# Performance work log

Measured on AMD Instinct MI355X. Metric: run time of the kernel, lower is better.

The kernel has to match this reference:

```python
import jax, jax.numpy as jnp
import numpy as np

N_NODES = 50000
N_EDGES = 625000
N_GRAPHS = 256
D = 128
STEPS = 3


def setup_inputs() -> dict:
    key = jax.random.key(0)
    ks = jax.random.split(key, 12)
    x = jax.random.normal(ks[0], (N_NODES, D), dtype=jnp.float32)
    edge_index = jax.random.randint(ks[1], (2, N_EDGES), 0, N_NODES, dtype=jnp.int64)
    batch = jnp.sort(jax.random.randint(ks[2], (N_NODES,), 0, N_GRAPHS, dtype=jnp.int64))
    s = 1.0 / np.sqrt(D)
    W1 = jax.random.uniform(ks[3], (D, D), jnp.float32, -s, s)
    b1 = jnp.zeros((D,), jnp.float32)
    W2 = jax.random.uniform(ks[4], (D, D), jnp.float32, -s, s)
    b2 = jnp.zeros((D,), jnp.float32)
    sh = 1.0 / np.sqrt(D)  # hidden size = D
    Wih = jax.random.uniform(ks[5], (4 * D, 2 * D), jnp.float32, -sh, sh)
    Whh = jax.random.uniform(ks[6], (4 * D, D), jnp.float32, -sh, sh)
    bih = jax.random.uniform(ks[7], (4 * D,), jnp.float32, -sh, sh)
    bhh = jax.random.uniform(ks[8], (4 * D,), jnp.float32, -sh, sh)
    return {"x": x, "edge_index": edge_index, "batch": batch,
            "W1": W1, "b1": b1, "W2": W2, "b2": b2,
            "Wih": Wih, "Whh": Whh, "bih": bih, "bhh": bhh}


def gcn_conv(x, edge_index, W, b):
    n = x.shape[0]
    src, dst = edge_index[0], edge_index[1]
    deg = jax.ops.segment_sum(jnp.ones(src.shape[0], x.dtype), dst, num_segments=n) + 1.0
    dinv = jax.lax.rsqrt(deg)
    xw = x @ W  # [N, out]
    norm = dinv[src] * dinv[dst]  # [E]
    agg = jax.ops.segment_sum(xw[src] * norm[:, None], dst, num_segments=n)
    agg = agg + xw * (dinv * dinv)[:, None]  # self-loop term (weight 1/deg_i)
    return agg + b


def set2set(x, batch, Wih, Whh, bih, bhh):
    d = x.shape[1]
    B = N_GRAPHS
    h = jnp.zeros((B, d), x.dtype)
    c = jnp.zeros((B, d), x.dtype)
    q_star = jnp.zeros((B, 2 * d), x.dtype)
    for _ in range(STEPS):
        # single-layer LSTM step (torch gate order: i, f, g, o)
        gates = q_star @ Wih.T + bih + h @ Whh.T + bhh
        i, f, g, o = jnp.split(gates, 4, axis=-1)
        c = jax.nn.sigmoid(f) * c + jax.nn.sigmoid(i) * jnp.tanh(g)
        h = jax.nn.sigmoid(o) * jnp.tanh(c)
        q = h  # [B, d]
        # attention with segment softmax over nodes grouped by graph
        e = jnp.sum(x * q[batch], axis=-1)  # [N]
        m = jax.ops.segment_max(e, batch, num_segments=B)
        m = jnp.where(jnp.isfinite(m), m, 0.0)  # guard empty graphs
        ex = jnp.exp(e - m[batch])
        ssum = jax.ops.segment_sum(ex, batch, num_segments=B)
        a = ex / (ssum[batch] + 1e-16)
        r = jax.ops.segment_sum(a[:, None] * x, batch, num_segments=B)  # [B, d]
        q_star = jnp.concatenate([q, r], axis=-1)
    return q_star  # [B, 2d]


def reference(x, edge_index, batch, W1, b1, W2, b2, Wih, Whh, bih, bhh):
    h1 = jax.nn.relu(gcn_conv(x, edge_index, W1, b1))
    h2 = gcn_conv(h1, edge_index, W2, b2)
    return set2set(h2, batch, Wih, Whh, bih, bhh)
```

## Files before the change

### kernel.cpp

```cpp
#include <hip/hip_runtime.h>
#include <hip/hip_fp16.h>
#include <math.h>

#define D 128

__device__ __forceinline__ float sigmoidf_(float x) { return 1.0f / (1.0f + expf(-x)); }

__global__ void k_deg(const int* __restrict__ dst, int* __restrict__ cnt, int E) {
    int i = blockIdx.x * blockDim.x + threadIdx.x;
    if (i < E) atomicAdd(&cnt[dst[i]], 1);
}

__global__ __launch_bounds__(256) void k_scan1(const int* __restrict__ cnt, int* __restrict__ row_ptr,
                                               int* __restrict__ bsum, float* __restrict__ dinv,
                                               int* __restrict__ fillc, int N) {
    __shared__ int sh[256];
    int t = threadIdx.x;
    int i = blockIdx.x * 256 + t;
    int v = (i < N) ? cnt[i] : 0;
    if (i < N) {
        dinv[i] = rsqrtf((float)v + 1.0f);
        fillc[i] = 0;
    }
    sh[t] = v;
    __syncthreads();
    for (int off = 1; off < 256; off <<= 1) {
        int u = (t >= off) ? sh[t - off] : 0;
        __syncthreads();
        sh[t] += u;
        __syncthreads();
    }
    if (i < N) row_ptr[i] = sh[t] - v;
    if (t == 255) bsum[blockIdx.x] = sh[255];
}

__global__ __launch_bounds__(256) void k_scan2(int* __restrict__ bsum, int nb,
                                               const int* __restrict__ batch, int* __restrict__ gstart,
                                               int N, int G) {
    __shared__ int sh[256];
    int t = threadIdx.x;
    int v = (t < nb) ? bsum[t] : 0;
    sh[t] = v;
    __syncthreads();
    for (int off = 1; off < 256; off <<= 1) {
        int u = (t >= off) ? sh[t - off] : 0;
        __syncthreads();
        sh[t] += u;
        __syncthreads();
    }
    if (t < nb) bsum[t] = sh[t] - v;
    for (int g = t; g <= G; g += 256) {
        int lo = 0, hi = N;
        while (lo < hi) {
            int mid = (lo + hi) >> 1;
            if (batch[mid] < g) lo = mid + 1; else hi = mid;
        }
        gstart[g] = lo;
    }
}

__global__ __launch_bounds__(256) void k_scan3(int* __restrict__ row_ptr, const int* __restrict__ bsum,
                                               int N, int E) {
    int i = blockIdx.x * 256 + threadIdx.x;
    if (i < N) row_ptr[i] += bsum[blockIdx.x];
    if (i == 0) row_ptr[N] = E;
}

__global__ void k_fill(const int* __restrict__ src, const int* __restrict__ dst,
                       const int* __restrict__ row_ptr, int* __restrict__ fillc,
                       int* __restrict__ s_sorted, int E) {
    int i = blockIdx.x * blockDim.x + threadIdx.x;
    if (i >= E) return;
    int s = src[i], d = dst[i];
    int pos = row_ptr[d] + atomicAdd(&fillc[d], 1);
    s_sorted[pos] = s;
}

__global__ __launch_bounds__(256) void k_prepw(const float* __restrict__ Wih, const float* __restrict__ Whh,
                                               float* __restrict__ Wcomb) {
    __shared__ float ta[32][33], tb[32][33];
    int t = threadIdx.x;
    int tx = t & 31, ty = t >> 5;
    int bk = blockIdx.x & 7, bj = blockIdx.x >> 3;
    int k0 = bk * 32, j0 = bj * 32;
    bool hh = (k0 < 128);
#pragma unroll
    for (int i = 0; i < 32; i += 8) ta[ty + i][tx] = Wih[(size_t)(j0 + ty + i) * 256 + k0 + tx];
    if (hh) {
#pragma unroll
        for (int i = 0; i < 32; i += 8) tb[ty + i][tx] = Whh[(size_t)(j0 + ty + i) * 128 + k0 + tx];
    }
    __syncthreads();
#pragma unroll
    for (int i = 0; i < 32; i += 8) {
        float v = ta[tx][ty + i];
        if (hh) v += tb[tx][ty + i];
        Wcomb[(size_t)(k0 + ty + i) * 512 + j0 + tx] = v;
    }
}

__global__ __launch_bounds__(256) void k_gemm(const float* __restrict__ X, const float* __restrict__ W,
                                              const float* __restrict__ dinv, __half* __restrict__ Y, int M) {
    __shared__ float Xs[32][68];
    __shared__ float Ws[32][128];
    int block_row = blockIdx.x * 64;
    int tid = threadIdx.x;
    int trr = tid >> 4;
    int tc = tid & 15;
    float acc[4][8] = {};
    for (int k0 = 0; k0 < 128; k0 += 32) {
        for (int i = tid; i < 512; i += 256) {
            int r = i >> 3, kk = (i & 7) << 2;
            int row = block_row + r;
            float4 v = make_float4(0.f, 0.f, 0.f, 0.f);
            if (row < M) v = *(const float4*)&X[(size_t)row * D + k0 + kk];
            Xs[kk + 0][r] = v.x; Xs[kk + 1][r] = v.y; Xs[kk + 2][r] = v.z; Xs[kk + 3][r] = v.w;
        }
        for (int i = tid; i < 1024; i += 256) {
            int r = i >> 5, cc = (i & 31) << 2;
            *(float4*)&Ws[r][cc] = *(const float4*)&W[(size_t)(k0 + r) * D + cc];
        }
        __syncthreads();
#pragma unroll
        for (int k = 0; k < 32; ++k) {
            float4 xv = *(const float4*)&Xs[k][trr * 4];
            float4 w0 = *(const float4*)&Ws[k][tc * 4];
            float4 w1 = *(const float4*)&Ws[k][tc * 4 + 64];
            float xr[4] = {xv.x, xv.y, xv.z, xv.w};
            float wc[8] = {w0.x, w0.y, w0.z, w0.w, w1.x, w1.y, w1.z, w1.w};
#pragma unroll
            for (int r = 0; r < 4; ++r)
#pragma unroll
                for (int c = 0; c < 8; ++c)
                    acc[r][c] += xr[r] * wc[c];
        }
        __syncthreads();
    }
    for (int r = 0; r < 4; ++r) {
        int row = block_row + trr * 4 + r;
        if (row < M) {
            float s = dinv[row];
            __half2* y0 = (__half2*)&Y[(size_t)row * D + tc * 4];
            y0[0] = __floats2half2_rn(acc[r][0] * s, acc[r][1] * s);
            y0[1] = __floats2half2_rn(acc[r][2] * s, acc[r][3] * s);
            __half2* y1 = (__half2*)&Y[(size_t)row * D + 64 + tc * 4];
            y1[0] = __floats2half2_rn(acc[r][4] * s, acc[r][5] * s);
            y1[1] = __floats2half2_rn(acc[r][6] * s, acc[r][7] * s);
        }
    }
}

template <bool RELU>
__global__ __launch_bounds__(256) void k_agg(const __half* __restrict__ xw, const int* __restrict__ s_sorted,
                                             const int* __restrict__ row_ptr, const float* __restrict__ dinv,
                                             const float* __restrict__ bias, float* __restrict__ out, int N) {
    int n = blockIdx.x * 4 + (threadIdx.x >> 6);
    if (n >= N) return;
    int l = threadIdx.x & 63;
    int beg = row_ptr[n], end = row_ptr[n + 1];
    float2 a[8];
#pragma unroll
    for (int k = 0; k < 8; ++k) a[k] = make_float2(0.f, 0.f);
    for (int e = beg; e < end; e += 8) {
#pragma unroll
        for (int k = 0; k < 8; ++k) {
            int idx = e + k;
            int ee = min(idx, end - 1);
            int s = s_sorted[ee];
            __half2 hv = *(const __half2*)&xw[(size_t)s * D + 2 * l];
            float2 xv = __half22float2(hv);
            bool ok = (idx < end);
            a[k].x += ok ? xv.x : 0.f;
            a[k].y += ok ? xv.y : 0.f;
        }
    }
    float din = dinv[n];
    __half2 hself = *(const __half2*)&xw[(size_t)n * D + 2 * l];
    float2 xs = __half22float2(hself);
    float2 bv = *(const float2*)&bias[2 * l];
    float sx = ((a[0].x + a[1].x) + (a[2].x + a[3].x)) + ((a[4].x + a[5].x) + (a[6].x + a[7].x));
    float sy = ((a[0].y + a[1].y) + (a[2].y + a[3].y)) + ((a[4].y + a[5].y) + (a[6].y + a[7].y));
    float rx = (sx + xs.x) * din + bv.x;
    float ry = (sy + xs.y) * din + bv.y;
    if (RELU) { rx = fmaxf(rx, 0.f); ry = fmaxf(ry, 0.f); }
    *(float2*)&out[(size_t)n * D + 2 * l] = make_float2(rx, ry);
}

__global__ __launch_bounds__(256) void k_lstm_gemm(const float* __restrict__ q_star,
                                                   const float* __restrict__ Wcomb,
                                                   float* __restrict__ gates) {
    __shared__ float Xs[32][68];
    __shared__ float Ws[32][64];
    int tid = threadIdx.x;
    int bm = blockIdx.x & 3, bn = blockIdx.x >> 2;
    int m0 = bm * 64, n0 = bn * 64;
    int trr = tid >> 4;
    int tc = tid & 15;
    float acc[4][4] = {};
    for (int k0 = 0; k0 < 256; k0 += 32) {
        for (int i = tid; i < 512; i += 256) {
            int r = i >> 3, kk = (i & 7) << 2;
            float4 v = *(const float4*)&q_star[(size_t)(m0 + r) * 256 + k0 + kk];
            Xs[kk + 0][r] = v.x; Xs[kk + 1][r] = v.y; Xs[kk + 2][r] = v.z; Xs[kk + 3][r] = v.w;
        }
        for (int i = tid; i < 512; i += 256) {
            int r = i >> 4, c = (i & 15) << 2;
            *(float4*)&Ws[r][c] = *(const float4*)&Wcomb[(size_t)(k0 + r) * 512 + n0 + c];
        }
        __syncthreads();
#pragma unroll
        for (int k = 0; k < 32; ++k) {
            float4 xv = *(const float4*)&Xs[k][trr * 4];
            float4 wv = *(const float4*)&Ws[k][tc * 4];
            float xr[4] = {xv.x, xv.y, xv.z, xv.w};
            float wc[4] = {wv.x, wv.y, wv.z, wv.w};
#pragma unroll
            for (int r = 0; r < 4; ++r)
#pragma unroll
                for (int c = 0; c < 4; ++c)
                    acc[r][c] += xr[r] * wc[c];
        }
        __syncthreads();
    }
#pragma unroll
    for (int r = 0; r < 4; ++r)
        *(float4*)&gates[(size_t)(m0 + trr * 4 + r) * 512 + n0 + tc * 4] =
            make_float4(acc[r][0], acc[r][1], acc[r][2], acc[r][3]);
}

template <bool FIRST>
__global__ __launch_bounds__(512) void k_attn2(const float* __restrict__ h2, const int* __restrict__ gstart,
                                               const float* __restrict__ gates, const float* __restrict__ bih,
                                               const float* __restrict__ bhh, float* __restrict__ c_all,
                                               float* __restrict__ q_star) {
    int g = blockIdx.x;
    int t = threadIdx.x;
    int wid = t >> 6, l = t & 63;
    int s = gstart[g], epos = gstart[g + 1];
    __shared__ float hs[D];
    __shared__ float wmax[8], wsum[8];
    __shared__ float2 racc2[512];
    if (t < D) {
        float ig = bih[t] + bhh[t];
        float fg = bih[t + D] + bhh[t + D];
        float gg = bih[t + 2 * D] + bhh[t + 2 * D];
        float og = bih[t + 3 * D] + bhh[t + 3 * D];
        if (!FIRST) {
            const float* gr = &gates[(size_t)g * 512];
            ig += gr[t]; fg += gr[t + D]; gg += gr[t + 2 * D]; og += gr[t + 3 * D];
        }
        float cprev = FIRST ? 0.f : c_all[g * D + t];
        float cc = sigmoidf_(fg) * cprev + sigmoidf_(ig) * tanhf(gg);
        float hh = sigmoidf_(og) * tanhf(cc);
        c_all[g * D + t] = cc;
        hs[t] = hh;
        q_star[(size_t)g * 2 * D + t] = hh;
    }
    __syncthreads();
    float2 qv = *(const float2*)&hs[2 * l];
    float m = -1e30f;
    float ssum = 0.f;
    float2 a = {0.f, 0.f};
    for (int i = s + wid * 4; i < epos; i += 32) {
        int i0 = i, i1 = min(i + 1, epos - 1), i2 = min(i + 2, epos - 1), i3 = min(i + 3, epos - 1);
        bool v1 = (i + 1 < epos), v2 = (i + 2 < epos), v3 = (i + 3 < epos);
        float2 x0 = *(const float2*)&h2[(size_t)i0 * D + 2 * l];
        float2 x1 = *(const float2*)&h2[(size_t)i1 * D + 2 * l];
        float2 x2 = *(const float2*)&h2[(size_t)i2 * D + 2 * l];
        float2 x3 = *(const float2*)&h2[(size_t)i3 * D + 2 * l];
        float d0 = x0.x * qv.x + x0.y * qv.y;
        float d1 = x1.x * qv.x + x1.y * qv.y;
        float d2 = x2.x * qv.x + x2.y * qv.y;
        float d3 = x3.x * qv.x + x3.y * qv.y;
#pragma unroll
        for (int off = 32; off; off >>= 1) {
            d0 += __shfl_xor(d0, off);
            d1 += __shfl_xor(d1, off);
            d2 += __shfl_xor(d2, off);
            d3 += __shfl_xor(d3, off);
        }
        {
            if (d0 > m) { float sc = expf(m - d0); a.x *= sc; a.y *= sc; ssum *= sc; m = d0; }
            float p = expf(d0 - m);
            ssum += p; a.x += p * x0.x; a.y += p * x0.y;
        }
        if (v1) {
            if (d1 > m) { float sc = expf(m - d1); a.x *= sc; a.y *= sc; ssum *= sc; m = d1; }
            float p = expf(d1 - m);
            ssum += p; a.x += p * x1.x; a.y += p * x1.y;
        }
        if (v2) {
            if (d2 > m) { float sc = expf(m - d2); a.x *= sc; a.y *= sc; ssum *= sc; m = d2; }
            float p = expf(d2 - m);
            ssum += p; a.x += p * x2.x; a.y += p * x2.y;
        }
        if (v3) {
            if (d3 > m) { float sc = expf(m - d3); a.x *= sc; a.y *= sc; ssum *= sc; m = d3; }
            float p = expf(d3 - m);
            ssum += p; a.x += p * x3.x; a.y += p * x3.y;
        }
    }
    if (l == 0) wmax[wid] = m;
    __syncthreads();
    float M = wmax[0];
#pragma unroll
    for (int w = 1; w < 8; ++w) M = fmaxf(M, wmax[w]);
    float fac = expf(m - M);
    a.x *= fac; a.y *= fac;
    ssum *= fac;
    if (l == 0) wsum[wid] = ssum;
    racc2[t] = a;
    __syncthreads();
    if (t < 64) {
        float S = 0.f;
#pragma unroll
        for (int w = 0; w < 8; ++w) S += wsum[w];
        float2 r = make_float2(0.f, 0.f);
#pragma unroll
        for (int w = 0; w < 8; ++w) { r.x += racc2[t + 64 * w].x; r.y += racc2[t + 64 * w].y; }
        float inv = 1.0f / (S + 1e-16f);
        q_star[(size_t)g * 2 * D + D + 2 * t] = r.x * inv;
        q_star[(size_t)g * 2 * D + D + 2 * t + 1] = r.y * inv;
    }
}

extern "C" void kernel_launch(void* const* d_in, const int* in_sizes, int n_in,
                              void* d_out, int out_size, void* d_ws, size_t ws_size,
                              hipStream_t stream) {
    const float* x = (const float*)d_in[0];
    const int* ei = (const int*)d_in[1];
    const int* batch = (const int*)d_in[2];
    const float* W1 = (const float*)d_in[3];
    const float* b1 = (const float*)d_in[4];
    const float* W2 = (const float*)d_in[5];
    const float* b2 = (const float*)d_in[6];
    const float* Wih = (const float*)d_in[7];
    const float* Whh = (const float*)d_in[8];
    const float* bih = (const float*)d_in[9];
    const float* bhh = (const float*)d_in[10];

    int N = in_sizes[2];
    int E = in_sizes[1] / 2;
    int G = out_size / (2 * D);
    const int* src = ei;
    const int* dst = ei + E;
    float* xbuf = (float*)d_in[0];
    float* q_star = (float*)d_out;

    float* wsf = (float*)d_ws;
    int* wsi = (int*)d_ws;
    size_t off = 0;
    float* dinv = wsf + off;    off += N;
    int* degcnt = wsi + off;    off += N;
    int* row_ptr = wsi + off;   off += N + 1;
    int* bsum = wsi + off;      off += 256;
    off = (off + 3) & ~(size_t)3;
    int* fillc = wsi + off;     off += N;
    int* s_sorted = wsi + off;  off += E;
    off = (off + 3) & ~(size_t)3;
    __half* bufA16 = (__half*)(wsf + off); off += (size_t)N * D / 2 + 4;
    int* gstart = wsi + off;    off += G + 1;
    off = (off + 3) & ~(size_t)3;
    float* Wcomb = wsf + off;   off += 256 * 512;
    float* gates = wsf + off;   off += (size_t)G * 512;
    float* c_all = wsf + off;   off += (size_t)G * D;

    hipMemsetAsync(degcnt, 0, N * sizeof(int), stream);

    int eb = (E + 255) / 256;
    int nb = (N + 255) / 256;
    k_deg<<<eb, 256, 0, stream>>>(dst, degcnt, E);
    k_scan1<<<nb, 256, 0, stream>>>(degcnt, row_ptr, bsum, dinv, fillc, N);
    k_scan2<<<1, 256, 0, stream>>>(bsum, nb, batch, gstart, N, G);
    k_scan3<<<nb, 256, 0, stream>>>(row_ptr, bsum, N, E);
    k_fill<<<eb, 256, 0, stream>>>(src, dst, row_ptr, fillc, s_sorted, E);
    k_prepw<<<128, 256, 0, stream>>>(Wih, Whh, Wcomb);

    int gb = (N + 63) / 64;
    k_gemm<<<gb, 256, 0, stream>>>(x, W1, dinv, bufA16, N);
    k_agg<true><<<(N + 3) / 4, 256, 0, stream>>>(bufA16, s_sorted, row_ptr, dinv, b1, xbuf, N);
    k_gemm<<<gb, 256, 0, stream>>>(xbuf, W2, dinv, bufA16, N);
    k_agg<false><<<(N + 3) / 4, 256, 0, stream>>>(bufA16, s_sorted, row_ptr, dinv, b2, xbuf, N);

    k_attn2<true><<<G, 512, 0, stream>>>(xbuf, gstart, gates, bih, bhh, c_all, q_star);
    for (int step = 1; step < 3; ++step) {
        k_lstm_gemm<<<32, 256, 0, stream>>>(q_star, Wcomb, gates);
        k_attn2<false><<<G, 512, 0, stream>>>(xbuf, gstart, gates, bih, bhh, c_all, q_star);
    }
}
```

Measured before the change: 350.7 us.

## Store hidden activations in fp16 and reuse atomic rank for CSR fill

```diff
diff --git a/kernel.cpp b/kernel.cpp
--- a/kernel.cpp
+++ b/kernel.cpp
@@ -6,22 +6,26 @@
 
 __device__ __forceinline__ float sigmoidf_(float x) { return 1.0f / (1.0f + expf(-x)); }
 
-__global__ void k_deg(const int* __restrict__ dst, int* __restrict__ cnt, int E) {
+__device__ __forceinline__ float4 load4(const float* p) { return *(const float4*)p; }
+__device__ __forceinline__ float4 load4(const __half* p) {
+    __half2 h0 = *(const __half2*)p;
+    __half2 h1 = *(const __half2*)(p + 2);
+    float2 f0 = __half22float2(h0), f1 = __half22float2(h1);
+    return make_float4(f0.x, f0.y, f1.x, f1.y);
+}
+
+__global__ void k_deg(const int* __restrict__ dst, int* __restrict__ cnt, int* __restrict__ rank, int E) {
     int i = blockIdx.x * blockDim.x + threadIdx.x;
-    if (i < E) atomicAdd(&cnt[dst[i]], 1);
+    if (i < E) rank[i] = atomicAdd(&cnt[dst[i]], 1);
 }
 
 __global__ __launch_bounds__(256) void k_scan1(const int* __restrict__ cnt, int* __restrict__ row_ptr,
-                                               int* __restrict__ bsum, float* __restrict__ dinv,
-                                               int* __restrict__ fillc, int N) {
+                                               int* __restrict__ bsum, float* __restrict__ dinv, int N) {
     __shared__ int sh[256];
     int t = threadIdx.x;
     int i = blockIdx.x * 256 + t;
     int v = (i < N) ? cnt[i] : 0;
-    if (i < N) {
-        dinv[i] = rsqrtf((float)v + 1.0f);
-        fillc[i] = 0;
-    }
+    if (i < N) dinv[i] = rsqrtf((float)v + 1.0f);
     sh[t] = v;
     __syncthreads();
     for (int off = 1; off < 256; off <<= 1) {
@@ -67,13 +71,11 @@
 }
 
 __global__ void k_fill(const int* __restrict__ src, const int* __restrict__ dst,
-                       const int* __restrict__ row_ptr, int* __restrict__ fillc,
+                       const int* __restrict__ row_ptr, const int* __restrict__ rank,
                        int* __restrict__ s_sorted, int E) {
     int i = blockIdx.x * blockDim.x + threadIdx.x;
     if (i >= E) return;
-    int s = src[i], d = dst[i];
-    int pos = row_ptr[d] + atomicAdd(&fillc[d], 1);
-    s_sorted[pos] = s;
+    s_sorted[row_ptr[dst[i]] + rank[i]] = src[i];
 }
 
 __global__ __launch_bounds__(256) void k_prepw(const float* __restrict__ Wih, const float* __restrict__ Whh,
@@ -99,7 +101,8 @@
     }
 }
 
-__global__ __launch_bounds__(256) void k_gemm(const float* __restrict__ X, const float* __restrict__ W,
+template <typename T>
+__global__ __launch_bounds__(256) void k_gemm(const T* __restrict__ X, const float* __restrict__ W,
                                               const float* __restrict__ dinv, __half* __restrict__ Y, int M) {
     __shared__ float Xs[32][68];
     __shared__ float Ws[32][128];
@@ -113,7 +116,7 @@
             int r = i >> 3, kk = (i & 7) << 2;
             int row = block_row + r;
             float4 v = make_float4(0.f, 0.f, 0.f, 0.f);
-            if (row < M) v = *(const float4*)&X[(size_t)row * D + k0 + kk];
+            if (row < M) v = load4(&X[(size_t)row * D + k0 + kk]);
             Xs[kk + 0][r] = v.x; Xs[kk + 1][r] = v.y; Xs[kk + 2][r] = v.z; Xs[kk + 3][r] = v.w;
         }
         for (int i = tid; i < 1024; i += 256) {
@@ -153,7 +156,7 @@
 template <bool RELU>
 __global__ __launch_bounds__(256) void k_agg(const __half* __restrict__ xw, const int* __restrict__ s_sorted,
                                              const int* __restrict__ row_ptr, const float* __restrict__ dinv,
-                                             const float* __restrict__ bias, float* __restrict__ out, int N) {
+                                             const float* __restrict__ bias, __half* __restrict__ out, int N) {
     int n = blockIdx.x * 4 + (threadIdx.x >> 6);
     if (n >= N) return;
     int l = threadIdx.x & 63;
@@ -175,15 +178,14 @@
         }
     }
     float din = dinv[n];
-    __half2 hself = *(const __half2*)&xw[(size_t)n * D + 2 * l];
-    float2 xs = __half22float2(hself);
+    float2 xs = __half22float2(*(const __half2*)&xw[(size_t)n * D + 2 * l]);
     float2 bv = *(const float2*)&bias[2 * l];
     float sx = ((a[0].x + a[1].x) + (a[2].x + a[3].x)) + ((a[4].x + a[5].x) + (a[6].x + a[7].x));
     float sy = ((a[0].y + a[1].y) + (a[2].y + a[3].y)) + ((a[4].y + a[5].y) + (a[6].y + a[7].y));
     float rx = (sx + xs.x) * din + bv.x;
     float ry = (sy + xs.y) * din + bv.y;
     if (RELU) { rx = fmaxf(rx, 0.f); ry = fmaxf(ry, 0.f); }
-    *(float2*)&out[(size_t)n * D + 2 * l] = make_float2(rx, ry);
+    *(__half2*)&out[(size_t)n * D + 2 * l] = __floats2half2_rn(rx, ry);
 }
 
 __global__ __launch_bounds__(256) void k_lstm_gemm(const float* __restrict__ q_star,
@@ -229,7 +231,7 @@
 }
 
 template <bool FIRST>
-__global__ __launch_bounds__(512) void k_attn2(const float* __restrict__ h2, const int* __restrict__ gstart,
+__global__ __launch_bounds__(512) void k_attn2(const __half* __restrict__ h2, const int* __restrict__ gstart,
                                                const float* __restrict__ gates, const float* __restrict__ bih,
                                                const float* __restrict__ bhh, float* __restrict__ c_all,
                                                float* __restrict__ q_star) {
@@ -264,10 +266,10 @@
     for (int i = s + wid * 4; i < epos; i += 32) {
         int i0 = i, i1 = min(i + 1, epos - 1), i2 = min(i + 2, epos - 1), i3 = min(i + 3, epos - 1);
         bool v1 = (i + 1 < epos), v2 = (i + 2 < epos), v3 = (i + 3 < epos);
-        float2 x0 = *(const float2*)&h2[(size_t)i0 * D + 2 * l];
-        float2 x1 = *(const float2*)&h2[(size_t)i1 * D + 2 * l];
-        float2 x2 = *(const float2*)&h2[(size_t)i2 * D + 2 * l];
-        float2 x3 = *(const float2*)&h2[(size_t)i3 * D + 2 * l];
+        float2 x0 = __half22float2(*(const __half2*)&h2[(size_t)i0 * D + 2 * l]);
+        float2 x1 = __half22float2(*(const __half2*)&h2[(size_t)i1 * D + 2 * l]);
+        float2 x2 = __half22float2(*(const __half2*)&h2[(size_t)i2 * D + 2 * l]);
+        float2 x3 = __half22float2(*(const __half2*)&h2[(size_t)i3 * D + 2 * l]);
         float d0 = x0.x * qv.x + x0.y * qv.y;
         float d1 = x1.x * qv.x + x1.y * qv.y;
         float d2 = x2.x * qv.x + x2.y * qv.y;
@@ -344,7 +346,6 @@
     int G = out_size / (2 * D);
     const int* src = ei;
     const int* dst = ei + E;
-    float* xbuf = (float*)d_in[0];
     float* q_star = (float*)d_out;
 
     float* wsf = (float*)d_ws;
@@ -355,10 +356,11 @@
     int* row_ptr = wsi + off;   off += N + 1;
     int* bsum = wsi + off;      off += 256;
     off = (off + 3) & ~(size_t)3;
-    int* fillc = wsi + off;     off += N;
+    int* rank = wsi + off;      off += E;
     int* s_sorted = wsi + off;  off += E;
     off = (off + 3) & ~(size_t)3;
     __half* bufA16 = (__half*)(wsf + off); off += (size_t)N * D / 2 + 4;
+    __half* h16 = (__half*)(wsf + off);    off += (size_t)N * D / 2 + 4;
     int* gstart = wsi + off;    off += G + 1;
     off = (off + 3) & ~(size_t)3;
     float* Wcomb = wsf + off;   off += 256 * 512;
@@ -369,22 +371,22 @@
 
     int eb = (E + 255) / 256;
     int nb = (N + 255) / 256;
-    k_deg<<<eb, 256, 0, stream>>>(dst, degcnt, E);
-    k_scan1<<<nb, 256, 0, stream>>>(degcnt, row_ptr, bsum, dinv, fillc, N);
+    k_deg<<<eb, 256, 0, stream>>>(dst, degcnt, rank, E);
+    k_scan1<<<nb, 256, 0, stream>>>(degcnt, row_ptr, bsum, dinv, N);
     k_scan2<<<1, 256, 0, stream>>>(bsum, nb, batch, gstart, N, G);
     k_scan3<<<nb, 256, 0, stream>>>(row_ptr, bsum, N, E);
-    k_fill<<<eb, 256, 0, stream>>>(src, dst, row_ptr, fillc, s_sorted, E);
+    k_fill<<<eb, 256, 0, stream>>>(src, dst, row_ptr, rank, s_sorted, E);
     k_prepw<<<128, 256, 0, stream>>>(Wih, Whh, Wcomb);
 
     int gb = (N + 63) / 64;
-    k_gemm<<<gb, 256, 0, stream>>>(x, W1, dinv, bufA16, N);
-    k_agg<true><<<(N + 3) / 4, 256, 0, stream>>>(bufA16, s_sorted, row_ptr, dinv, b1, xbuf, N);
-    k_gemm<<<gb, 256, 0, stream>>>(xbuf, W2, dinv, bufA16, N);
-    k_agg<false><<<(N + 3) / 4, 256, 0, stream>>>(bufA16, s_sorted, row_ptr, dinv, b2, xbuf, N);
-
-    k_attn2<true><<<G, 512, 0, stream>>>(xbuf, gstart, gates, bih, bhh, c_all, q_star);
+    k_gemm<float><<<gb, 256, 0, stream>>>(x, W1, dinv, bufA16, N);
+    k_agg<true><<<(N + 3) / 4, 256, 0, stream>>>(bufA16, s_sorted, row_ptr, dinv, b1, h16, N);
+    k_gemm<__half><<<gb, 256, 0, stream>>>(h16, W2, dinv, bufA16, N);
+    k_agg<false><<<(N + 3) / 4, 256, 0, stream>>>(bufA16, s_sorted, row_ptr, dinv, b2, h16, N);
+
+    k_attn2<true><<<G, 512, 0, stream>>>(h16, gstart, gates, bih, bhh, c_all, q_star);
     for (int step = 1; step < 3; ++step) {
         k_lstm_gemm<<<32, 256, 0, stream>>>(q_star, Wcomb, gates);
-        k_attn2<false><<<G, 512, 0, stream>>>(xbuf, gstart, gates, bih, bhh, c_all, q_star);
-    }
-}
+        k_attn2<false><<<G, 512, 0, stream>>>(h16, gstart, gates, bih, bhh, c_all, q_star);
+    }
+}
```

Result: faster. 327.3 us (-6.7%).
